# Performance work log

Measured on AMD Instinct MI355X. Metric: run time of the kernel, lower is better.

Reference implementation:

```python
import jax, jax.numpy as jnp
import numpy as np

EPS = 1e-12
NEG_INF = -1e30

def _slog(x):
    return jnp.log(jnp.clip(x, EPS))

def setup_inputs() -> dict:
    M, Z = 24, 1024
    key = jax.random.key(0)
    ks = jax.random.split(key, 20)
    u = lambda k, sh, s=1.0: jax.random.uniform(k, sh, dtype=jnp.float32) * s
    demin = u(ks[0], (M, M), 0.2)
    demax = demin + u(ks[1], (M, M), 1.0)
    Kn = (jax.random.uniform(ks[2], (M, M)) > 0.5).astype(jnp.float32)
    # a couple of sectors with no substitution choices (rows stay all-ones in S)
    Kn = Kn.at[0].set(0.0).at[5].set(0.0)
    housing_mask = jnp.zeros((M,), dtype=bool).at[jnp.array([M - 2, M - 1])].set(True)
    genflux_mask = (jax.random.uniform(ks[3], (M,)) > 0.2)
    return {
        'h': jnp.zeros((M, Z), jnp.float32),
        'price': u(ks[4], (M, Z)),
        't_nij': u(ks[5], (M, Z, Z)),
        'demin': demin,
        'demax': demax,
        'delta': u(ks[6], (M, M), 0.2),
        'omega': u(ks[7], (M, M)),
        'sigma': u(ks[8], (M,), 0.5),
        'Kn': Kn,
        'attractor': u(ks[9], (M, Z)) + 0.1,
        'beta': u(ks[10], (M,), 0.5),
        'lamda': u(ks[11], (M,)),
        'A_ni': u(ks[12], (M, Z)) + 0.1,
        'exog_demand': u(ks[13], (M, Z)),
        'exog_prod': u(ks[14], (M, Z)),
        'X_0': u(ks[15], (M, Z)) + 0.1,
        'X_target': u(ks[16], (M, Z)),
        'housing_mask': housing_mask,
        'genflux_mask': genflux_mask,
    }

def reference(h, price, t_nij, demin, demax, delta, omega, sigma, Kn,
              attractor, beta, lamda, A_ni, exog_demand, exog_prod,
              X_0, X_target, housing_mask, genflux_mask):
    M, Z = price.shape
    ph = price + h                                            # [n,i] prices + shadow prices
    # LocationProbability: U_nij = lamda_n*ph[n,j] + t_nij; Pr = softmax_j for genflux non-housing, else eye
    U_nij = lamda[:, None, None] * ph[:, None, :] + t_nij     # [n,i,j]
    loc_logits = _slog(A_ni)[:, None, :] - beta[:, None, None] * U_nij
    Pr_soft = jax.nn.softmax(loc_logits, axis=-1)
    loc_mask = genflux_mask & (~housing_mask)                 # sectors with location choice
    eye = jnp.eye(Z, dtype=price.dtype)
    Pr = jnp.where(loc_mask[:, None, None], Pr_soft, eye[None, :, :])  # [n,i,j]
    # composite (expected) disutility per sector/zone
    U_ni = jnp.einsum('nij,nij->ni', Pr, U_nij)               # [n,i]
    # DemandFunction: a[m,n,i] = demin + (demax-demin)*exp(-delta*U_ni)
    a_mni = demin[:, :, None] + (demax - demin)[:, :, None] * jnp.exp(-delta[:, :, None] * U_ni[None])
    # SubstitutionProbability: masked softmax over substitutes n (axis=1), S=1 where no choice
    U_tilde = omega[:, :, None] * a_mni * U_ni[None]          # [m,n,i]
    cmask = (Kn > 0)[:, :, None]                              # [m,n,1]
    sub_logits = jnp.where(cmask, _slog(attractor)[None] - sigma[:, None, None] * U_tilde, NEG_INF)
    S_mni = jnp.where(cmask, jax.nn.softmax(sub_logits, axis=1), 1.0)
    # TotalDemand: D[n,i] = exog_demand + sum_m a*S*(X_0+exog_prod)
    X_total = X_0 + exog_prod
    D_ni = exog_demand + jnp.einsum('mni,mni,mi->ni', a_mni, S_mni, X_total)
    # induced production: X_pred[n,j] = sum_i D[n,i] * Pr[n,i,j]
    X_pred = jnp.einsum('ni,nij->nj', D_ni, Pr)
    return jnp.mean((X_pred - X_target) ** 2)
```

## Files before the change

kernel.cpp:

```cpp
#include <hip/hip_runtime.h>
#include <hip/hip_bf16.h>
#include <math.h>

#define MDIM 24
#define ZDIM 1024
#define NEG_INF_F -1e30f
#define EPS_F 1e-12f

enum {
  OFF_U    = 0,
  OFF_RMAX = 24576,
  OFF_SEXP = 49152,
  OFF_W    = 73728,
  OFF_XP   = 98304
};

__device__ __forceinline__ bool masks_are_bytes(const void* hm, const void* gm) {
  const unsigned int* hw = (const unsigned int*)hm;
  const unsigned int* gw = (const unsigned int*)gm;
  bool b = false;
  #pragma unroll
  for (int k = 0; k < 6; k++) {
    unsigned int a = hw[k], c = gw[k];
    if (a != 0u && a != 1u && a != 0x3F800000u) b = true;
    if (c != 0u && c != 1u && c != 0x3F800000u) b = true;
  }
  return b;
}
__device__ __forceinline__ bool loc_flag(const void* hm, const void* gm, int n) {
  bool bytes = masks_are_bytes(hm, gm);
  bool hv = bytes ? (((const unsigned char*)hm)[n] != 0)
                  : (((const unsigned int*)hm)[n] != 0u);
  bool gv = bytes ? (((const unsigned char*)gm)[n] != 0)
                  : (((const unsigned int*)gm)[n] != 0u);
  return gv && !hv;
}

__global__ __launch_bounds__(256) void k1_rows(
    const float* __restrict__ t, const float* __restrict__ price,
    const float* __restrict__ h, const float* __restrict__ A_ni,
    const float* __restrict__ beta, const float* __restrict__ lamda,
    const void* __restrict__ housing, const void* __restrict__ genflux,
    float* __restrict__ ws) {
  const int n  = blockIdx.x >> 6;
  const int i0 = (blockIdx.x & 63) * 16;
  const float bn = beta[n], ln = lamda[n];
  const bool lf = loc_flag(housing, genflux, n);
  if (!lf) {
    if (threadIdx.x < 16) {
      const int row = n * ZDIM + i0 + threadIdx.x;
      ws[OFF_U + row] = ln * (price[row] + h[row])
                        + t[(size_t)row * ZDIM + (i0 + threadIdx.x)];
    }
    return;
  }
  __shared__ float pc_s[ZDIM];
  __shared__ float cc_s[ZDIM];
  for (int j = threadIdx.x; j < ZDIM; j += 256) {
    const float pc = ln * (price[n * ZDIM + j] + h[n * ZDIM + j]);
    const float sa = logf(fmaxf(A_ni[n * ZDIM + j], EPS_F));
    pc_s[j] = pc;
    cc_s[j] = sa - bn * pc;
  }
  __syncthreads();
  const int wave = threadIdx.x >> 6, lane = threadIdx.x & 63;
  const float4* pc4 = (const float4*)pc_s;
  const float4* cc4 = (const float4*)cc_s;

  auto do_row = [&](int row, float4 t0, float4 t1, float4 t2, float4 t3) {
    float lg[16], uv[16];
    float mx = -INFINITY;
    const float4 tt[4] = {t0, t1, t2, t3};
    #pragma unroll
    for (int k = 0; k < 4; k++) {
      const int f = lane + 64 * k;
      const float4 tv = tt[k];
      const float4 pv = pc4[f];
      const float4 cv = cc4[f];
      uv[4*k+0] = pv.x + tv.x;  lg[4*k+0] = cv.x - bn * tv.x;
      uv[4*k+1] = pv.y + tv.y;  lg[4*k+1] = cv.y - bn * tv.y;
      uv[4*k+2] = pv.z + tv.z;  lg[4*k+2] = cv.z - bn * tv.z;
      uv[4*k+3] = pv.w + tv.w;  lg[4*k+3] = cv.w - bn * tv.w;
      mx = fmaxf(mx, fmaxf(fmaxf(lg[4*k], lg[4*k+1]), fmaxf(lg[4*k+2], lg[4*k+3])));
    }
    #pragma unroll
    for (int off = 32; off >= 1; off >>= 1)
      mx = fmaxf(mx, __shfl_xor(mx, off));
    float se = 0.f, su = 0.f;
    #pragma unroll
    for (int k = 0; k < 16; k++) {
      const float e = __expf(lg[k] - mx);
      se += e;
      su = fmaf(e, uv[k], su);
    }
    #pragma unroll
    for (int off = 32; off >= 1; off >>= 1) {
      se += __shfl_xor(se, off);
      su += __shfl_xor(su, off);
    }
    if (lane == 0) {
      ws[OFF_U + row]    = su / se;
      ws[OFF_RMAX + row] = mx;
      ws[OFF_SEXP + row] = se;
    }
  };

  #pragma unroll
  for (int p = 0; p < 2; p++) {
    const int rA = n * ZDIM + i0 + wave * 4 + p * 2;
    const int rB = rA + 1;
    const float4* tA = (const float4*)(t + (size_t)rA * ZDIM);
    const float4* tB = (const float4*)(t + (size_t)rB * ZDIM);
    const float4 a0 = tA[lane], a1 = tA[lane + 64],
                 a2 = tA[lane + 128], a3 = tA[lane + 192];
    const float4 b0 = tB[lane], b1 = tB[lane + 64],
                 b2 = tB[lane + 128], b3 = tB[lane + 192];
    do_row(rA, a0, a1, a2, a3);
    do_row(rB, b0, b1, b2, b3);
  }
}

__global__ __launch_bounds__(256) void k2_demand(
    const float* __restrict__ demin, const float* __restrict__ demax,
    const float* __restrict__ delta, const float* __restrict__ omega,
    const float* __restrict__ sigma, const float* __restrict__ Kn,
    const float* __restrict__ attractor, const float* __restrict__ exogd,
    const float* __restrict__ X0, const float* __restrict__ exogp,
    const void* __restrict__ housing, const void* __restrict__ genflux,
    float* __restrict__ ws) {
  const int wave = threadIdx.x >> 6;
  const int lane = threadIdx.x & 63;
  const int half = lane >> 5;
  const int n    = lane & 31;
  const int i    = blockIdx.x * 8 + wave * 2 + half;
  const bool nv  = (n < MDIM);
  float Uv = 0.f, asl = NEG_INF_F;
  if (nv) {
    Uv  = ws[OFF_U + n * ZDIM + i];
    asl = logf(fmaxf(attractor[n * ZDIM + i], EPS_F));
  }
  float acc = 0.f;
  for (int m = 0; m < MDIM; m++) {
    const float Xt  = X0[m * ZDIM + i] + exogp[m * ZDIM + i];
    const float sig = sigma[m];
    float dm = 0.f, dd = 0.f, dl = 0.f, om = 0.f, kn = 0.f;
    if (nv) {
      dm = demin[m * MDIM + n];
      dd = demax[m * MDIM + n] - dm;
      dl = delta[m * MDIM + n];
      om = omega[m * MDIM + n];
      kn = Kn[m * MDIM + n];
    }
    const float a = dm + dd * __expf(-dl * Uv);
    const bool valid = nv && (kn > 0.f);
    const float l = valid ? asl - sig * om * a * Uv : NEG_INF_F;
    float mx = l;
    #pragma unroll
    for (int off = 16; off >= 1; off >>= 1)
      mx = fmaxf(mx, __shfl_xor(mx, off));
    const float e = valid ? __expf(l - mx) : 0.f;
    float se = e;
    #pragma unroll
    for (int off = 16; off >= 1; off >>= 1)
      se += __shfl_xor(se, off);
    const float S = (valid && se > 0.f) ? e / se : 1.0f;
    if (nv) acc = fmaf(a * S, Xt, acc);
  }
  if (nv) {
    const float Dv = exogd[n * ZDIM + i] + acc;
    if (loc_flag(housing, genflux, n)) {
      ws[OFF_W  + n * ZDIM + i] = Dv / ws[OFF_SEXP + n * ZDIM + i];
      ws[OFF_XP + n * ZDIM + i] = 0.f;
    } else {
      ws[OFF_XP + n * ZDIM + i] = Dv;
    }
  }
}

__global__ __launch_bounds__(256) void k3_xpred(
    const float* __restrict__ t, const float* __restrict__ price,
    const float* __restrict__ h, const float* __restrict__ A_ni,
    const float* __restrict__ beta, const float* __restrict__ lamda,
    const void* __restrict__ housing, const void* __restrict__ genflux,
    float* __restrict__ ws) {
  const int n = blockIdx.x >> 6, ic = blockIdx.x & 63;
  if (!loc_flag(housing, genflux, n)) return;
  const int tj = threadIdx.x;
  const float bn = beta[n], ln = lamda[n];
  const float4 pr = ((const float4*)(price + n * ZDIM))[tj];
  const float4 hh = ((const float4*)(h     + n * ZDIM))[tj];
  const float4 aa = ((const float4*)(A_ni  + n * ZDIM))[tj];
  const float c0 = logf(fmaxf(aa.x, EPS_F)) - bn * (ln * (pr.x + hh.x));
  const float c1 = logf(fmaxf(aa.y, EPS_F)) - bn * (ln * (pr.y + hh.y));
  const float c2 = logf(fmaxf(aa.z, EPS_F)) - bn * (ln * (pr.z + hh.z));
  const float c3 = logf(fmaxf(aa.w, EPS_F)) - bn * (ln * (pr.w + hh.w));
  const float4* t4 = (const float4*)t;
  int row = n * ZDIM + ic * 16;
  float  mx_c = ws[OFF_RMAX + row];
  float  w_c  = ws[OFF_W + row];
  float4 tv_c = t4[(size_t)row * (ZDIM / 4) + tj];
  float x0 = 0.f, x1 = 0.f, x2 = 0.f, x3 = 0.f;
  for (int ii = 0; ii < 16; ii++) {
    float mx_n = 0.f, w_n = 0.f;
    float4 tv_n = tv_c;
    if (ii < 15) {
      mx_n = ws[OFF_RMAX + row + 1];
      w_n  = ws[OFF_W + row + 1];
      tv_n = t4[(size_t)(row + 1) * (ZDIM / 4) + tj];
    }
    x0 = fmaf(w_c, __expf(c0 - mx_c - bn * tv_c.x), x0);
    x1 = fmaf(w_c, __expf(c1 - mx_c - bn * tv_c.y), x1);
    x2 = fmaf(w_c, __expf(c2 - mx_c - bn * tv_c.z), x2);
    x3 = fmaf(w_c, __expf(c3 - mx_c - bn * tv_c.w), x3);
    mx_c = mx_n; w_c = w_n; tv_c = tv_n; row++;
  }
  float* xp = ws + OFF_XP + n * ZDIM + tj * 4;
  atomicAdd(xp + 0, x0);
  atomicAdd(xp + 1, x1);
  atomicAdd(xp + 2, x2);
  atomicAdd(xp + 3, x3);
}

__global__ __launch_bounds__(256) void k4_loss(
    const float* __restrict__ Xtg, const float* __restrict__ ws,
    float* __restrict__ out) {
  float s = 0.f;
  for (int e = blockIdx.x * 256 + threadIdx.x; e < MDIM * ZDIM; e += 48 * 256) {
    const float d = ws[OFF_XP + e] - Xtg[e];
    s = fmaf(d, d, s);
  }
  #pragma unroll
  for (int off = 32; off >= 1; off >>= 1) s += __shfl_xor(s, off);
  __shared__ float red[4];
  const int w = threadIdx.x >> 6, lane = threadIdx.x & 63;
  if (lane == 0) red[w] = s;
  __syncthreads();
  if (threadIdx.x == 0)
    atomicAdd(out, (red[0] + red[1] + red[2] + red[3]) * (1.0f / (MDIM * ZDIM)));
}

extern "C" void kernel_launch(void* const* d_in, const int* in_sizes, int n_in,
                              void* d_out, int out_size, void* d_ws, size_t ws_size,
                              hipStream_t stream) {
  (void)in_sizes; (void)n_in; (void)out_size; (void)ws_size;
  const float* h       = (const float*)d_in[0];
  const float* price   = (const float*)d_in[1];
  const float* t       = (const float*)d_in[2];
  const float* demin   = (const float*)d_in[3];
  const float* demax   = (const float*)d_in[4];
  const float* delta   = (const float*)d_in[5];
  const float* omega   = (const float*)d_in[6];
  const float* sigma   = (const float*)d_in[7];
  const float* Kn      = (const float*)d_in[8];
  const float* attract = (const float*)d_in[9];
  const float* beta    = (const float*)d_in[10];
  const float* lamda   = (const float*)d_in[11];
  const float* A_ni    = (const float*)d_in[12];
  const float* exogd   = (const float*)d_in[13];
  const float* exogp   = (const float*)d_in[14];
  const float* X0      = (const float*)d_in[15];
  const float* Xtg     = (const float*)d_in[16];
  const void*  housing = d_in[17];
  const void*  genflux = d_in[18];
  float* ws  = (float*)d_ws;
  float* out = (float*)d_out;

  k1_rows<<<MDIM * 64, 256, 0, stream>>>(t, price, h, A_ni, beta, lamda,
                                         housing, genflux, ws);
  k2_demand<<<128, 256, 0, stream>>>(demin, demax, delta, omega, sigma, Kn,
                                     attract, exogd, X0, exogp,
                                     housing, genflux, ws);
  k3_xpred<<<MDIM * 64, 256, 0, stream>>>(t, price, h, A_ni, beta, lamda,
                                          housing, genflux, ws);
  hipMemsetAsync(out, 0, sizeof(float), stream);
  k4_loss<<<48, 256, 0, stream>>>(Xtg, ws, out);
}
```

Before: 237.8 us.

## Deepen load prefetch in row kernels and single-block loss without memset

k1 now issues the loads for all four of a wave's t rows before any compute, where it previously loaded two rows at a time. k3 gets a 4-deep rotating prefetch buffer for t rows and row stats in a fully unrolled loop, replacing the single-row lookahead. The loss kernel becomes one 1024-thread block that writes the result directly, which removes the memset and the atomics. The aim is more memory-level parallelism on the bandwidth-bound t streams at the cost of higher register pressure, plus one fewer launch at the end.

```diff
diff --git a/kernel.cpp b/kernel.cpp
--- a/kernel.cpp
+++ b/kernel.cpp
@@ -45,8 +45,7 @@
   const int n  = blockIdx.x >> 6;
   const int i0 = (blockIdx.x & 63) * 16;
   const float bn = beta[n], ln = lamda[n];
-  const bool lf = loc_flag(housing, genflux, n);
-  if (!lf) {
+  if (!loc_flag(housing, genflux, n)) {
     if (threadIdx.x < 16) {
       const int row = n * ZDIM + i0 + threadIdx.x;
       ws[OFF_U + row] = ln * (price[row] + h[row])
@@ -66,21 +65,32 @@
   const int wave = threadIdx.x >> 6, lane = threadIdx.x & 63;
   const float4* pc4 = (const float4*)pc_s;
   const float4* cc4 = (const float4*)cc_s;
-
-  auto do_row = [&](int row, float4 t0, float4 t1, float4 t2, float4 t3) {
+  const int r0 = n * ZDIM + i0 + wave * 4;
+
+  float4 tv[4][4];
+  #pragma unroll
+  for (int r = 0; r < 4; r++) {
+    const float4* tp = (const float4*)(t + (size_t)(r0 + r) * ZDIM);
+    tv[r][0] = tp[lane];
+    tv[r][1] = tp[lane + 64];
+    tv[r][2] = tp[lane + 128];
+    tv[r][3] = tp[lane + 192];
+  }
+
+  #pragma unroll
+  for (int r = 0; r < 4; r++) {
     float lg[16], uv[16];
     float mx = -INFINITY;
-    const float4 tt[4] = {t0, t1, t2, t3};
     #pragma unroll
     for (int k = 0; k < 4; k++) {
       const int f = lane + 64 * k;
-      const float4 tv = tt[k];
+      const float4 tt = tv[r][k];
       const float4 pv = pc4[f];
       const float4 cv = cc4[f];
-      uv[4*k+0] = pv.x + tv.x;  lg[4*k+0] = cv.x - bn * tv.x;
-      uv[4*k+1] = pv.y + tv.y;  lg[4*k+1] = cv.y - bn * tv.y;
-      uv[4*k+2] = pv.z + tv.z;  lg[4*k+2] = cv.z - bn * tv.z;
-      uv[4*k+3] = pv.w + tv.w;  lg[4*k+3] = cv.w - bn * tv.w;
+      uv[4*k+0] = pv.x + tt.x;  lg[4*k+0] = cv.x - bn * tt.x;
+      uv[4*k+1] = pv.y + tt.y;  lg[4*k+1] = cv.y - bn * tt.y;
+      uv[4*k+2] = pv.z + tt.z;  lg[4*k+2] = cv.z - bn * tt.z;
+      uv[4*k+3] = pv.w + tt.w;  lg[4*k+3] = cv.w - bn * tt.w;
       mx = fmaxf(mx, fmaxf(fmaxf(lg[4*k], lg[4*k+1]), fmaxf(lg[4*k+2], lg[4*k+3])));
     }
     #pragma unroll
@@ -99,24 +109,11 @@
       su += __shfl_xor(su, off);
     }
     if (lane == 0) {
+      const int row = r0 + r;
       ws[OFF_U + row]    = su / se;
       ws[OFF_RMAX + row] = mx;
       ws[OFF_SEXP + row] = se;
     }
-  };
-
-  #pragma unroll
-  for (int p = 0; p < 2; p++) {
-    const int rA = n * ZDIM + i0 + wave * 4 + p * 2;
-    const int rB = rA + 1;
-    const float4* tA = (const float4*)(t + (size_t)rA * ZDIM);
-    const float4* tB = (const float4*)(t + (size_t)rB * ZDIM);
-    const float4 a0 = tA[lane], a1 = tA[lane + 64],
-                 a2 = tA[lane + 128], a3 = tA[lane + 192];
-    const float4 b0 = tB[lane], b1 = tB[lane + 64],
-                 b2 = tB[lane + 128], b3 = tB[lane + 192];
-    do_row(rA, a0, a1, a2, a3);
-    do_row(rB, b0, b1, b2, b3);
   }
 }
 
@@ -195,24 +192,30 @@
   const float c2 = logf(fmaxf(aa.z, EPS_F)) - bn * (ln * (pr.z + hh.z));
   const float c3 = logf(fmaxf(aa.w, EPS_F)) - bn * (ln * (pr.w + hh.w));
   const float4* t4 = (const float4*)t;
-  int row = n * ZDIM + ic * 16;
-  float  mx_c = ws[OFF_RMAX + row];
-  float  w_c  = ws[OFF_W + row];
-  float4 tv_c = t4[(size_t)row * (ZDIM / 4) + tj];
+  const int base = n * ZDIM + ic * 16;
+  float4 tv[4];
+  float  mx[4], w[4];
+  #pragma unroll
+  for (int r = 0; r < 4; r++) {
+    tv[r] = t4[(size_t)(base + r) * (ZDIM / 4) + tj];
+    mx[r] = ws[OFF_RMAX + base + r];
+    w[r]  = ws[OFF_W + base + r];
+  }
   float x0 = 0.f, x1 = 0.f, x2 = 0.f, x3 = 0.f;
+  #pragma unroll
   for (int ii = 0; ii < 16; ii++) {
-    float mx_n = 0.f, w_n = 0.f;
-    float4 tv_n = tv_c;
-    if (ii < 15) {
-      mx_n = ws[OFF_RMAX + row + 1];
-      w_n  = ws[OFF_W + row + 1];
-      tv_n = t4[(size_t)(row + 1) * (ZDIM / 4) + tj];
-    }
-    x0 = fmaf(w_c, __expf(c0 - mx_c - bn * tv_c.x), x0);
-    x1 = fmaf(w_c, __expf(c1 - mx_c - bn * tv_c.y), x1);
-    x2 = fmaf(w_c, __expf(c2 - mx_c - bn * tv_c.z), x2);
-    x3 = fmaf(w_c, __expf(c3 - mx_c - bn * tv_c.w), x3);
-    mx_c = mx_n; w_c = w_n; tv_c = tv_n; row++;
+    const int s = ii & 3;
+    const float4 cv = tv[s];
+    const float  m  = mx[s], wt = w[s];
+    if (ii < 12) {
+      tv[s] = t4[(size_t)(base + ii + 4) * (ZDIM / 4) + tj];
+      mx[s] = ws[OFF_RMAX + base + ii + 4];
+      w[s]  = ws[OFF_W + base + ii + 4];
+    }
+    x0 = fmaf(wt, __expf(c0 - m - bn * cv.x), x0);
+    x1 = fmaf(wt, __expf(c1 - m - bn * cv.y), x1);
+    x2 = fmaf(wt, __expf(c2 - m - bn * cv.z), x2);
+    x3 = fmaf(wt, __expf(c3 - m - bn * cv.w), x3);
   }
   float* xp = ws + OFF_XP + n * ZDIM + tj * 4;
   atomicAdd(xp + 0, x0);
@@ -221,22 +224,26 @@
   atomicAdd(xp + 3, x3);
 }
 
-__global__ __launch_bounds__(256) void k4_loss(
+__global__ __launch_bounds__(1024) void k4_loss(
     const float* __restrict__ Xtg, const float* __restrict__ ws,
     float* __restrict__ out) {
   float s = 0.f;
-  for (int e = blockIdx.x * 256 + threadIdx.x; e < MDIM * ZDIM; e += 48 * 256) {
+  for (int e = threadIdx.x; e < MDIM * ZDIM; e += 1024) {
     const float d = ws[OFF_XP + e] - Xtg[e];
     s = fmaf(d, d, s);
   }
   #pragma unroll
   for (int off = 32; off >= 1; off >>= 1) s += __shfl_xor(s, off);
-  __shared__ float red[4];
+  __shared__ float red[16];
   const int w = threadIdx.x >> 6, lane = threadIdx.x & 63;
   if (lane == 0) red[w] = s;
   __syncthreads();
-  if (threadIdx.x == 0)
-    atomicAdd(out, (red[0] + red[1] + red[2] + red[3]) * (1.0f / (MDIM * ZDIM)));
+  if (threadIdx.x == 0) {
+    float tot = 0.f;
+    #pragma unroll
+    for (int k = 0; k < 16; k++) tot += red[k];
+    *out = tot * (1.0f / (MDIM * ZDIM));
+  }
 }
 
 extern "C" void kernel_launch(void* const* d_in, const int* in_sizes, int n_in,
@@ -272,6 +279,5 @@
                                      housing, genflux, ws);
   k3_xpred<<<MDIM * 64, 256, 0, stream>>>(t, price, h, A_ni, beta, lamda,
                                           housing, genflux, ws);
-  hipMemsetAsync(out, 0, sizeof(float), stream);
-  k4_loss<<<48, 256, 0, stream>>>(Xtg, ws, out);
-}
+  k4_loss<<<1, 1024, 0, stream>>>(Xtg, ws, out);
+}
```

Result: slower. 248.8 us (+4.6%).
